# Kernel tuning notes

Measured on AMD Instinct MI355X. Metric: run time of the kernel, lower is better.

## Reference

```python
import jax, jax.numpy as jnp
import numpy as np

N_NODES = 100000
N_HYPEREDGES = 20000
NNZ = 600000
D = 128


def setup_inputs() -> dict:
    key = jax.random.key(0)
    k = jax.random.split(key, 6)
    s = 1.0 / np.sqrt(D)
    x = jax.random.normal(k[0], (N_NODES, D), jnp.float32)
    node_idx = jax.random.randint(k[1], (NNZ,), 0, N_NODES, dtype=jnp.int64 if jax.config.jax_enable_x64 else jnp.int32)
    edge_idx = jax.random.randint(k[2], (NNZ,), 0, N_HYPEREDGES, dtype=jnp.int64 if jax.config.jax_enable_x64 else jnp.int32)
    conv_W = jax.random.uniform(k[3], (D, D), jnp.float32, -s, s)
    conv_b = jnp.zeros((D,), jnp.float32)
    res_W = jax.random.uniform(k[4], (D, D), jnp.float32, -s, s)
    res_b = jax.random.uniform(k[5], (D,), jnp.float32, -s, s)
    return {"x": x, "node_idx": node_idx, "edge_idx": edge_idx,
            "conv_W": conv_W, "conv_b": conv_b, "res_W": res_W, "res_b": res_b}


def hypergraph_conv(x, node_idx, edge_idx, W, b):
    # PyG HypergraphConv (no attention, unit hyperedge weights):
    #   out = D^{-1} H B^{-1} H^T (x W) + b
    y = x @ W                                                      # [N, D]
    ones = jnp.ones(node_idx.shape, dtype=y.dtype)
    deg_n = jax.ops.segment_sum(ones, node_idx, num_segments=N_NODES)        # node degree
    deg_e = jax.ops.segment_sum(ones, edge_idx, num_segments=N_HYPEREDGES)   # hyperedge size
    inv_n = jnp.where(deg_n > 0, 1.0 / deg_n, 0.0)
    inv_e = jnp.where(deg_e > 0, 1.0 / deg_e, 0.0)
    # node -> hyperedge aggregation, normalized by B^{-1}
    e_feat = jax.ops.segment_sum(y[node_idx], edge_idx, num_segments=N_HYPEREDGES)
    e_feat = e_feat * inv_e[:, None]                               # [E, D]
    # hyperedge -> node aggregation, normalized by D^{-1}
    out = jax.ops.segment_sum(e_feat[edge_idx], node_idx, num_segments=N_NODES)
    out = out * inv_n[:, None]                                     # [N, D]
    return out + b


def reference(x, node_idx, edge_idx, conv_W, conv_b, res_W, res_b):
    h = hypergraph_conv(x, node_idx, edge_idx, conv_W, conv_b)     # layer_num = 1
    return (x @ res_W + res_b) + h                                 # residual Linear + conv out
```

## Files before the change

kernel.cpp:

```cpp
#include <hip/hip_runtime.h>

#define N_NODES 100000
#define N_EDGES 20000
#define NNZ_C   600000
#define D 128

typedef short bf16x8 __attribute__((ext_vector_type(8)));
typedef float f32x4  __attribute__((ext_vector_type(4)));

__device__ __forceinline__ unsigned short f2bf(float f) {
    unsigned int u = __float_as_uint(f);
    u = (u + 0x7fffu + ((u >> 16) & 1u)) >> 16;
    return (unsigned short)u;
}
__device__ __forceinline__ float bf2f(unsigned short h) {
    return __uint_as_float((unsigned int)h << 16);
}
__device__ __forceinline__ unsigned int pk_trunc(float lo, float hi) {
    return __builtin_amdgcn_perm(__float_as_uint(hi), __float_as_uint(lo),
                                 0x07060302);
}

#define CH 4096
#define NCHUNK 147
#define CONVB 256
#define EBW 32
#define NBE 625
#define ECAP 1280
#define NBW 128
#define NBN 782
#define NCAP 1024
#define PADI 32
#define GCUR_INTS ((NBE + NBN) * PADI)

#define GT 64
#define XPAD 136
#define NTILES ((N_NODES + GT - 1) / GT)

__global__ __launch_bounds__(512) void fused_bin_conv(
    const float* __restrict__ x,
    const int* __restrict__ nidx, const int* __restrict__ eidx,
    unsigned short* __restrict__ xb,
    int* __restrict__ bucket_e, int* __restrict__ bucket_n,
    int* __restrict__ gcur_e, int* __restrict__ gcur_n) {
    __shared__ int srt[CH];
    __shared__ int cnt[NBN], lbase[NBN], gbase[NBN], cur[NBN];
    const int bid = blockIdx.x;
    const int tid = threadIdx.x;

    if (bid >= NCHUNK) {
        const int total8 = N_NODES * D / 8;
        for (int g = (bid - NCHUNK) * 512 + tid; g < total8;
             g += CONVB * 512) {
            const float4 a = *(const float4*)(x + (size_t)g * 8);
            const float4 c = *(const float4*)(x + (size_t)g * 8 + 4);
            uint4 v;
            v.x = pk_trunc(a.x, a.y);
            v.y = pk_trunc(a.z, a.w);
            v.z = pk_trunc(c.x, c.y);
            v.w = pk_trunc(c.z, c.w);
            *(uint4*)(xb + (size_t)g * 8) = v;
        }
        return;
    }

    const int j0 = bid * CH;
    const int jn = (j0 + CH < NNZ_C) ? CH : NNZ_C - j0;
#pragma unroll
    for (int s = 0; s < 2; ++s) {
        const int nb = s ? NBN : NBE;
        int* gc = s ? gcur_n : gcur_e;
        int* dst = s ? bucket_n : bucket_e;
        const int cap = s ? NCAP : ECAP;
        for (int i = tid; i < nb; i += 512) cnt[i] = 0;
        __syncthreads();
        for (int i = tid; i < jn; i += 512) {
            const int id = s ? nidx[j0 + i] : eidx[j0 + i];
            atomicAdd(&cnt[s ? (id >> 7) : (id >> 5)], 1);
        }
        __syncthreads();
        if (tid < 64) {
            int loc[13];
            int ssum = 0;
            const int k0 = tid * 13;
#pragma unroll
            for (int k = 0; k < 13; ++k) {
                const int idx = k0 + k;
                loc[k] = ssum;
                if (idx < nb) ssum += cnt[idx];
            }
            int v = ssum;
#pragma unroll
            for (int off = 1; off < 64; off <<= 1) {
                const int t = __shfl_up(v, off);
                if (tid >= off) v += t;
            }
            const int base = v - ssum;
#pragma unroll
            for (int k = 0; k < 13; ++k) {
                const int idx = k0 + k;
                if (idx < nb) {
                    lbase[idx] = base + loc[k];
                    cur[idx] = base + loc[k];
                }
            }
        }
        __syncthreads();
        for (int i = tid; i < nb; i += 512)
            gbase[i] = cnt[i] ? atomicAdd(&gc[i * PADI], cnt[i]) : 0;
        __syncthreads();
        for (int i = tid; i < jn; i += 512) {
            const int e = eidx[j0 + i], n = nidx[j0 + i];
            const int b = s ? (n >> 7) : (e >> 5);
            const unsigned pk = s ? (unsigned)(((n & 127) << 15) | e)
                                  : (unsigned)(((e & 31) << 17) | n);
            const int pos = atomicAdd(&cur[b], 1);
            srt[pos] = (int)(pk | ((unsigned)b << 22));
        }
        __syncthreads();
        for (int i = tid; i < jn; i += 512) {
            const unsigned v = (unsigned)srt[i];
            const int b = v >> 22;
            const int o2 = gbase[b] + (i - lbase[b]);
            if (o2 < cap) dst[b * cap + o2] = (int)(v & 0x3FFFFFu);
        }
        __syncthreads();
    }
}

__global__ __launch_bounds__(512) void edge_mean(
    const int* __restrict__ bucket_e, const int* __restrict__ gcur_e,
    const unsigned short* __restrict__ xb, unsigned short* __restrict__ sb) {
    __shared__ int raw[ECAP];
    __shared__ int srt[ECAP];
    __shared__ int cnt[EBW + 1];
    __shared__ int cur[EBW];
    const int tid = threadIdx.x;
    const int b = blockIdx.x;
    int W = gcur_e[b * PADI];
    if (W > ECAP) W = ECAP;
    if (tid <= EBW) cnt[tid] = 0;
    __syncthreads();
    const int* src = bucket_e + b * ECAP;
    for (int i = tid; i < W; i += 512) {
        const int p = src[i];
        raw[i] = p;
        atomicAdd(&cnt[p >> 17], 1);
    }
    __syncthreads();
    if (tid < EBW) {
        const int c = cnt[tid];
        int v = c;
#pragma unroll
        for (int off = 1; off < EBW; off <<= 1) {
            const int t = __shfl_up(v, off);
            if (tid >= off) v += t;
        }
        cnt[tid] = v - c;
        cur[tid] = v - c;
        if (tid == EBW - 1) cnt[EBW] = v;
    }
    __syncthreads();
    for (int i = tid; i < W; i += 512) {
        const int p = raw[i];
        const int pos = atomicAdd(&cur[p >> 17], 1);
        srt[pos] = p & 0x1FFFF;
    }
    __syncthreads();

    const int g = tid >> 4;
    const int l = tid & 15;
    const int beg = cnt[g], end = cnt[g + 1];
    float acc[8] = {};
    int j = beg;
    for (; j + 8 <= end; j += 8) {
        bf16x8 p[8];
#pragma unroll
        for (int q = 0; q < 8; ++q)
            p[q] = *(const bf16x8*)(xb + (size_t)srt[j + q] * D + l * 8);
#pragma unroll
        for (int i = 0; i < 8; ++i) {
            float t0 = bf2f((unsigned short)p[0][i]) + bf2f((unsigned short)p[1][i]);
            float t1 = bf2f((unsigned short)p[2][i]) + bf2f((unsigned short)p[3][i]);
            float t2 = bf2f((unsigned short)p[4][i]) + bf2f((unsigned short)p[5][i]);
            float t3 = bf2f((unsigned short)p[6][i]) + bf2f((unsigned short)p[7][i]);
            acc[i] += (t0 + t1) + (t2 + t3);
        }
    }
    for (; j + 4 <= end; j += 4) {
        const int n0 = srt[j], n1 = srt[j + 1];
        const int n2 = srt[j + 2], n3 = srt[j + 3];
        const bf16x8 p0 = *(const bf16x8*)(xb + (size_t)n0 * D + l * 8);
        const bf16x8 p1 = *(const bf16x8*)(xb + (size_t)n1 * D + l * 8);
        const bf16x8 p2 = *(const bf16x8*)(xb + (size_t)n2 * D + l * 8);
        const bf16x8 p3 = *(const bf16x8*)(xb + (size_t)n3 * D + l * 8);
#pragma unroll
        for (int i = 0; i < 8; ++i)
            acc[i] += (bf2f((unsigned short)p0[i]) + bf2f((unsigned short)p1[i]))
                    + (bf2f((unsigned short)p2[i]) + bf2f((unsigned short)p3[i]));
    }
    for (; j < end; ++j) {
        const bf16x8 p = *(const bf16x8*)(xb + (size_t)srt[j] * D + l * 8);
#pragma unroll
        for (int i = 0; i < 8; ++i) acc[i] += bf2f((unsigned short)p[i]);
    }
    const int deg = end - beg;
    const float inv = deg ? 1.f / (float)deg : 0.f;
    bf16x8 o;
#pragma unroll
    for (int i = 0; i < 8; ++i) o[i] = (short)f2bf(acc[i] * inv);
    *(bf16x8*)(sb + (size_t)(b * EBW + g) * D + l * 8) = o;
}

__global__ __launch_bounds__(512, 4) void node_gemm(
    const int* __restrict__ bucket_n, const int* __restrict__ gcur_n,
    const unsigned short* __restrict__ sb, const unsigned short* __restrict__ xb,
    const float* __restrict__ cW, const float* __restrict__ rW,
    const float* __restrict__ cbias, const float* __restrict__ rbias,
    float* __restrict__ out) {
    __shared__ int raw[NCAP];
    __shared__ int srt[NCAP];
    __shared__ int cnt[NBW + 1];
    __shared__ int cur[NBW];
    __shared__ unsigned short zs[NBW * XPAD];
    __shared__ unsigned short xs[GT * XPAD];
    const int tid = threadIdx.x;
    const int b = blockIdx.x;

    int W = gcur_n[b * PADI];
    if (W > NCAP) W = NCAP;
    if (tid <= NBW) cnt[tid] = 0;
    __syncthreads();
    const int* src = bucket_n + b * NCAP;
    for (int i = tid; i < W; i += 512) {
        const int p = src[i];
        raw[i] = p;
        atomicAdd(&cnt[p >> 15], 1);
    }
    __syncthreads();
    if (tid < 64) {
        const int a0 = cnt[tid * 2], a1 = cnt[tid * 2 + 1];
        const int ssum = a0 + a1;
        int v = ssum;
#pragma unroll
        for (int off = 1; off < 64; off <<= 1) {
            const int t = __shfl_up(v, off);
            if (tid >= off) v += t;
        }
        const int base = v - ssum;
        cnt[tid * 2] = base;          cur[tid * 2] = base;
        cnt[tid * 2 + 1] = base + a0; cur[tid * 2 + 1] = base + a0;
        if (tid == 63) cnt[NBW] = v;
    }
    __syncthreads();
    for (int i = tid; i < W; i += 512) {
        const int p = raw[i];
        const int pos = atomicAdd(&cur[p >> 15], 1);
        srt[pos] = p & 0x7FFF;
    }
    __syncthreads();

    {
        const int g = tid >> 4;
        const int l = tid & 15;
#pragma unroll
        for (int u = 0; u < 4; ++u) {
            const int nl = g * 4 + u;
            const int beg = cnt[nl], end = cnt[nl + 1];
            float acc[8] = {};
            int j = beg;
            for (; j + 4 <= end; j += 4) {
                const int e0 = srt[j], e1 = srt[j + 1];
                const int e2 = srt[j + 2], e3 = srt[j + 3];
                const bf16x8 p0 = *(const bf16x8*)(sb + (size_t)e0 * D + l * 8);
                const bf16x8 p1 = *(const bf16x8*)(sb + (size_t)e1 * D + l * 8);
                const bf16x8 p2 = *(const bf16x8*)(sb + (size_t)e2 * D + l * 8);
                const bf16x8 p3 = *(const bf16x8*)(sb + (size_t)e3 * D + l * 8);
#pragma unroll
                for (int i = 0; i < 8; ++i)
                    acc[i] += (bf2f((unsigned short)p0[i]) + bf2f((unsigned short)p1[i]))
                            + (bf2f((unsigned short)p2[i]) + bf2f((unsigned short)p3[i]));
            }
            for (; j < end; ++j) {
                const bf16x8 p = *(const bf16x8*)(sb + (size_t)srt[j] * D + l * 8);
#pragma unroll
                for (int i = 0; i < 8; ++i) acc[i] += bf2f((unsigned short)p[i]);
            }
            const int deg = end - beg;
            const float inv = deg ? 1.f / (float)deg : 0.f;
            bf16x8 o;
#pragma unroll
            for (int i = 0; i < 8; ++i) o[i] = (short)f2bf(acc[i] * inv);
            *(bf16x8*)(zs + nl * XPAD + l * 8) = o;
        }
    }

    const int w    = tid >> 6;
    const int lane = tid & 63;
    const int quad = lane >> 4;
    const int l16  = lane & 15;
    const int f0   = w * 16;
    const int f    = f0 + l16;
    bf16x8 Ac[4], Ar[4];
#pragma unroll
    for (int kc = 0; kc < 4; ++kc)
#pragma unroll
        for (int u = 0; u < 8; ++u) {
            const int k = kc * 32 + quad * 8 + u;
            Ac[kc][u] = (short)f2bf(cW[(size_t)k * D + f]);
            Ar[kc][u] = (short)f2bf(rW[(size_t)k * D + f]);
        }
    const float4 cb4 = *(const float4*)(cbias + f0 + quad * 4);
    const float4 rb4 = *(const float4*)(rbias + f0 + quad * 4);
    const float4 bias = {cb4.x + rb4.x, cb4.y + rb4.y,
                         cb4.z + rb4.z, cb4.w + rb4.w};

    const int r0 = tid >> 3;
    const int qp = tid & 7;

#pragma unroll
    for (int h = 0; h < 2; ++h) {
        __syncthreads();
        {
            int n = b * NBW + h * GT + r0;
            if (n >= N_NODES) n = N_NODES - 1;
            const uint4* sx = (const uint4*)(xb + (size_t)n * D + qp * 16);
            uint4* dx = (uint4*)(xs + r0 * XPAD + qp * 16);
            dx[0] = sx[0]; dx[1] = sx[1];
        }
        __syncthreads();
        f32x4 acc[4] = {};
#pragma unroll
        for (int g = 0; g < 4; ++g)
#pragma unroll
            for (int kc = 0; kc < 4; ++kc) {
                const int ko = kc * 32 + quad * 8;
                const bf16x8 Bz = *(const bf16x8*)(zs + (h * GT + g * 16 + l16) * XPAD + ko);
                const bf16x8 Bx = *(const bf16x8*)(xs + (g * 16 + l16) * XPAD + ko);
                acc[g] = __builtin_amdgcn_mfma_f32_16x16x32_bf16(Ac[kc], Bz, acc[g], 0, 0, 0);
                acc[g] = __builtin_amdgcn_mfma_f32_16x16x32_bf16(Ar[kc], Bx, acc[g], 0, 0, 0);
            }
#pragma unroll
        for (int g = 0; g < 4; ++g) {
            const int n = b * NBW + h * GT + g * 16 + l16;
            if (n >= N_NODES) continue;
            float4 o;
            o.x = acc[g][0] + bias.x;
            o.y = acc[g][1] + bias.y;
            o.z = acc[g][2] + bias.z;
            o.w = acc[g][3] + bias.w;
            *(float4*)(out + (size_t)n * D + f0 + quad * 4) = o;
        }
    }
}

extern "C" void kernel_launch(void* const* d_in, const int* in_sizes, int n_in,
                              void* d_out, int out_size, void* d_ws,
                              size_t ws_size, hipStream_t stream) {
    const float* x  = (const float*)d_in[0];
    const int* nidx = (const int*)d_in[1];
    const int* eidx = (const int*)d_in[2];
    const float* cW = (const float*)d_in[3];
    const float* cb = (const float*)d_in[4];
    const float* rW = (const float*)d_in[5];
    const float* rb = (const float*)d_in[6];
    float* out = (float*)d_out;

    char* ws = (char*)d_ws;
    size_t off = 0;
    auto alloc = [&](size_t bytes) {
        size_t o = off;
        off += (bytes + 255) & ~(size_t)255;
        return o;
    };
    unsigned short* xb = (unsigned short*)(ws + alloc((size_t)N_NODES * D * 2));
    unsigned short* sb = (unsigned short*)(ws + alloc((size_t)N_EDGES * D * 2));
    int* bucket_e = (int*)(ws + alloc((size_t)NBE * ECAP * 4));
    int* bucket_n = (int*)(ws + alloc((size_t)NBN * NCAP * 4));
    int* gcur     = (int*)(ws + alloc((size_t)GCUR_INTS * 4));
    int* gcur_e = gcur;
    int* gcur_n = gcur + NBE * PADI;

    hipMemsetAsync(gcur, 0, (size_t)GCUR_INTS * 4, stream);

    fused_bin_conv<<<NCHUNK + CONVB, 512, 0, stream>>>(
        x, nidx, eidx, xb, bucket_e, bucket_n, gcur_e, gcur_n);

    edge_mean<<<NBE, 512, 0, stream>>>(bucket_e, gcur_e, xb, sb);
    node_gemm<<<NBN, 512, 0, stream>>>(bucket_n, gcur_n, sb, xb,
                                       cW, rW, cb, rb, out);
}
```

Baseline: 190.7 us.

## Halve bucket widths, pre-transpose bf16 weights, drop LDS raw staging

Bucket widths are halved: 16 hyperedges per edge bucket and 64 nodes per node bucket. This doubles the number of blocks in edge_mean and node_gemm, gives more parallelism and smaller LDS footprints, and lets node_gemm process a single 64-row tile. Extra blocks in the fused binning kernel convert and transpose both weight matrices to bf16 once, so each node_gemm block loads its MFMA A fragments with vector loads instead of 64 strided scalar fp32 loads. The raw LDS staging of bucket entries is removed, and bucket entries are re-read from global memory instead. The costs are a second global read of bucket data, more blocks re-loading weights, and tighter per-bucket capacities that risk truncation.

```diff
diff --git a/kernel.cpp b/kernel.cpp
--- a/kernel.cpp
+++ b/kernel.cpp
@@ -24,23 +24,27 @@
 #define CH 4096
 #define NCHUNK 147
 #define CONVB 256
-#define EBW 32
-#define NBE 625
-#define ECAP 1280
-#define NBW 128
-#define NBN 782
-#define NCAP 1024
+#define WBLK 8
+#define EBW 16
+#define NBE 1250
+#define ECAP 768
+#define NBW 64
+#define NBN 1563
+#define NCAP 640
 #define PADI 32
 #define GCUR_INTS ((NBE + NBN) * PADI)
+#define TAGSH 21
+#define PKMASK 0x1FFFFF
 
 #define GT 64
 #define XPAD 136
-#define NTILES ((N_NODES + GT - 1) / GT)
 
 __global__ __launch_bounds__(512) void fused_bin_conv(
     const float* __restrict__ x,
     const int* __restrict__ nidx, const int* __restrict__ eidx,
+    const float* __restrict__ cW, const float* __restrict__ rW,
     unsigned short* __restrict__ xb,
+    unsigned short* __restrict__ wtc, unsigned short* __restrict__ wtr,
     int* __restrict__ bucket_e, int* __restrict__ bucket_n,
     int* __restrict__ gcur_e, int* __restrict__ gcur_n) {
     __shared__ int srt[CH];
@@ -48,6 +52,18 @@
     const int bid = blockIdx.x;
     const int tid = threadIdx.x;
 
+    if (bid >= NCHUNK + CONVB) {
+        const int t0 = (bid - NCHUNK - CONVB) * 4096;
+        for (int i = tid; i < 4096; i += 512) {
+            const int t = t0 + i;
+            const int m = t >> 14, idx = t & 16383;
+            const int f = idx & 127, k = idx >> 7;
+            const float* src = m ? rW : cW;
+            unsigned short* dst = m ? wtr : wtc;
+            dst[f * D + k] = f2bf(src[k * D + f]);
+        }
+        return;
+    }
     if (bid >= NCHUNK) {
         const int total8 = N_NODES * D / 8;
         for (int g = (bid - NCHUNK) * 512 + tid; g < total8;
@@ -76,15 +92,15 @@
         __syncthreads();
         for (int i = tid; i < jn; i += 512) {
             const int id = s ? nidx[j0 + i] : eidx[j0 + i];
-            atomicAdd(&cnt[s ? (id >> 7) : (id >> 5)], 1);
+            atomicAdd(&cnt[s ? (id >> 6) : (id >> 4)], 1);
         }
         __syncthreads();
         if (tid < 64) {
-            int loc[13];
+            int loc[25];
             int ssum = 0;
-            const int k0 = tid * 13;
-#pragma unroll
-            for (int k = 0; k < 13; ++k) {
+            const int k0 = tid * 25;
+#pragma unroll
+            for (int k = 0; k < 25; ++k) {
                 const int idx = k0 + k;
                 loc[k] = ssum;
                 if (idx < nb) ssum += cnt[idx];
@@ -97,7 +113,7 @@
             }
             const int base = v - ssum;
 #pragma unroll
-            for (int k = 0; k < 13; ++k) {
+            for (int k = 0; k < 25; ++k) {
                 const int idx = k0 + k;
                 if (idx < nb) {
                     lbase[idx] = base + loc[k];
@@ -111,27 +127,26 @@
         __syncthreads();
         for (int i = tid; i < jn; i += 512) {
             const int e = eidx[j0 + i], n = nidx[j0 + i];
-            const int b = s ? (n >> 7) : (e >> 5);
-            const unsigned pk = s ? (unsigned)(((n & 127) << 15) | e)
-                                  : (unsigned)(((e & 31) << 17) | n);
+            const int b = s ? (n >> 6) : (e >> 4);
+            const unsigned pk = s ? (unsigned)(((n & 63) << 15) | e)
+                                  : (unsigned)(((e & 15) << 17) | n);
             const int pos = atomicAdd(&cur[b], 1);
-            srt[pos] = (int)(pk | ((unsigned)b << 22));
+            srt[pos] = (int)(pk | ((unsigned)b << TAGSH));
         }
         __syncthreads();
         for (int i = tid; i < jn; i += 512) {
             const unsigned v = (unsigned)srt[i];
-            const int b = v >> 22;
+            const int b = (int)(v >> TAGSH);
             const int o2 = gbase[b] + (i - lbase[b]);
-            if (o2 < cap) dst[b * cap + o2] = (int)(v & 0x3FFFFFu);
-        }
-        __syncthreads();
-    }
-}
-
-__global__ __launch_bounds__(512) void edge_mean(
+            if (o2 < cap) dst[b * cap + o2] = (int)(v & PKMASK);
+        }
+        __syncthreads();
+    }
+}
+
+__global__ __launch_bounds__(256) void edge_mean(
     const int* __restrict__ bucket_e, const int* __restrict__ gcur_e,
     const unsigned short* __restrict__ xb, unsigned short* __restrict__ sb) {
-    __shared__ int raw[ECAP];
     __shared__ int srt[ECAP];
     __shared__ int cnt[EBW + 1];
     __shared__ int cur[EBW];
@@ -142,11 +157,8 @@
     if (tid <= EBW) cnt[tid] = 0;
     __syncthreads();
     const int* src = bucket_e + b * ECAP;
-    for (int i = tid; i < W; i += 512) {
-        const int p = src[i];
-        raw[i] = p;
-        atomicAdd(&cnt[p >> 17], 1);
-    }
+    for (int i = tid; i < W; i += 256)
+        atomicAdd(&cnt[src[i] >> 17], 1);
     __syncthreads();
     if (tid < EBW) {
         const int c = cnt[tid];
@@ -161,8 +173,8 @@
         if (tid == EBW - 1) cnt[EBW] = v;
     }
     __syncthreads();
-    for (int i = tid; i < W; i += 512) {
-        const int p = raw[i];
+    for (int i = tid; i < W; i += 256) {
+        const int p = src[i];
         const int pos = atomicAdd(&cur[p >> 17], 1);
         srt[pos] = p & 0x1FFFF;
     }
@@ -215,10 +227,9 @@
 __global__ __launch_bounds__(512, 4) void node_gemm(
     const int* __restrict__ bucket_n, const int* __restrict__ gcur_n,
     const unsigned short* __restrict__ sb, const unsigned short* __restrict__ xb,
-    const float* __restrict__ cW, const float* __restrict__ rW,
+    const unsigned short* __restrict__ wtc, const unsigned short* __restrict__ wtr,
     const float* __restrict__ cbias, const float* __restrict__ rbias,
     float* __restrict__ out) {
-    __shared__ int raw[NCAP];
     __shared__ int srt[NCAP];
     __shared__ int cnt[NBW + 1];
     __shared__ int cur[NBW];
@@ -232,29 +243,24 @@
     if (tid <= NBW) cnt[tid] = 0;
     __syncthreads();
     const int* src = bucket_n + b * NCAP;
-    for (int i = tid; i < W; i += 512) {
-        const int p = src[i];
-        raw[i] = p;
-        atomicAdd(&cnt[p >> 15], 1);
-    }
+    for (int i = tid; i < W; i += 512)
+        atomicAdd(&cnt[src[i] >> 15], 1);
     __syncthreads();
     if (tid < 64) {
-        const int a0 = cnt[tid * 2], a1 = cnt[tid * 2 + 1];
-        const int ssum = a0 + a1;
-        int v = ssum;
+        const int c = cnt[tid];
+        int v = c;
 #pragma unroll
         for (int off = 1; off < 64; off <<= 1) {
             const int t = __shfl_up(v, off);
             if (tid >= off) v += t;
         }
-        const int base = v - ssum;
-        cnt[tid * 2] = base;          cur[tid * 2] = base;
-        cnt[tid * 2 + 1] = base + a0; cur[tid * 2 + 1] = base + a0;
+        cnt[tid] = v - c;
+        cur[tid] = v - c;
         if (tid == 63) cnt[NBW] = v;
     }
     __syncthreads();
     for (int i = tid; i < W; i += 512) {
-        const int p = raw[i];
+        const int p = src[i];
         const int pos = atomicAdd(&cur[p >> 15], 1);
         srt[pos] = p & 0x7FFF;
     }
@@ -264,8 +270,8 @@
         const int g = tid >> 4;
         const int l = tid & 15;
 #pragma unroll
-        for (int u = 0; u < 4; ++u) {
-            const int nl = g * 4 + u;
+        for (int u = 0; u < 2; ++u) {
+            const int nl = g * 2 + u;
             const int beg = cnt[nl], end = cnt[nl + 1];
             float acc[8] = {};
             int j = beg;
@@ -303,54 +309,46 @@
     const int f    = f0 + l16;
     bf16x8 Ac[4], Ar[4];
 #pragma unroll
-    for (int kc = 0; kc < 4; ++kc)
-#pragma unroll
-        for (int u = 0; u < 8; ++u) {
-            const int k = kc * 32 + quad * 8 + u;
-            Ac[kc][u] = (short)f2bf(cW[(size_t)k * D + f]);
-            Ar[kc][u] = (short)f2bf(rW[(size_t)k * D + f]);
-        }
+    for (int kc = 0; kc < 4; ++kc) {
+        Ac[kc] = *(const bf16x8*)(wtc + (size_t)f * D + kc * 32 + quad * 8);
+        Ar[kc] = *(const bf16x8*)(wtr + (size_t)f * D + kc * 32 + quad * 8);
+    }
     const float4 cb4 = *(const float4*)(cbias + f0 + quad * 4);
     const float4 rb4 = *(const float4*)(rbias + f0 + quad * 4);
     const float4 bias = {cb4.x + rb4.x, cb4.y + rb4.y,
                          cb4.z + rb4.z, cb4.w + rb4.w};
 
-    const int r0 = tid >> 3;
-    const int qp = tid & 7;
-
-#pragma unroll
-    for (int h = 0; h < 2; ++h) {
-        __syncthreads();
-        {
-            int n = b * NBW + h * GT + r0;
-            if (n >= N_NODES) n = N_NODES - 1;
-            const uint4* sx = (const uint4*)(xb + (size_t)n * D + qp * 16);
-            uint4* dx = (uint4*)(xs + r0 * XPAD + qp * 16);
-            dx[0] = sx[0]; dx[1] = sx[1];
-        }
-        __syncthreads();
-        f32x4 acc[4] = {};
-#pragma unroll
-        for (int g = 0; g < 4; ++g)
-#pragma unroll
-            for (int kc = 0; kc < 4; ++kc) {
-                const int ko = kc * 32 + quad * 8;
-                const bf16x8 Bz = *(const bf16x8*)(zs + (h * GT + g * 16 + l16) * XPAD + ko);
-                const bf16x8 Bx = *(const bf16x8*)(xs + (g * 16 + l16) * XPAD + ko);
-                acc[g] = __builtin_amdgcn_mfma_f32_16x16x32_bf16(Ac[kc], Bz, acc[g], 0, 0, 0);
-                acc[g] = __builtin_amdgcn_mfma_f32_16x16x32_bf16(Ar[kc], Bx, acc[g], 0, 0, 0);
-            }
-#pragma unroll
-        for (int g = 0; g < 4; ++g) {
-            const int n = b * NBW + h * GT + g * 16 + l16;
-            if (n >= N_NODES) continue;
-            float4 o;
-            o.x = acc[g][0] + bias.x;
-            o.y = acc[g][1] + bias.y;
-            o.z = acc[g][2] + bias.z;
-            o.w = acc[g][3] + bias.w;
-            *(float4*)(out + (size_t)n * D + f0 + quad * 4) = o;
-        }
+    {
+        const int r0 = tid >> 3;
+        const int qp = tid & 7;
+        int n = b * NBW + r0;
+        if (n >= N_NODES) n = N_NODES - 1;
+        const uint4* sx = (const uint4*)(xb + (size_t)n * D + qp * 16);
+        uint4* dx = (uint4*)(xs + r0 * XPAD + qp * 16);
+        dx[0] = sx[0]; dx[1] = sx[1];
+    }
+    __syncthreads();
+    f32x4 acc[4] = {};
+#pragma unroll
+    for (int g = 0; g < 4; ++g)
+#pragma unroll
+        for (int kc = 0; kc < 4; ++kc) {
+            const int ro = (g * 16 + l16) * XPAD + kc * 32 + quad * 8;
+            const bf16x8 Bz = *(const bf16x8*)(zs + ro);
+            const bf16x8 Bx = *(const bf16x8*)(xs + ro);
+            acc[g] = __builtin_amdgcn_mfma_f32_16x16x32_bf16(Ac[kc], Bz, acc[g], 0, 0, 0);
+            acc[g] = __builtin_amdgcn_mfma_f32_16x16x32_bf16(Ar[kc], Bx, acc[g], 0, 0, 0);
+        }
+#pragma unroll
+    for (int g = 0; g < 4; ++g) {
+        const int n = b * NBW + g * 16 + l16;
+        if (n >= N_NODES) continue;
+        float4 o;
+        o.x = acc[g][0] + bias.x;
+        o.y = acc[g][1] + bias.y;
+        o.z = acc[g][2] + bias.z;
+        o.w = acc[g][3] + bias.w;
+        *(float4*)(out + (size_t)n * D + f0 + quad * 4) = o;
     }
 }
 
@@ -373,8 +371,10 @@
         off += (bytes + 255) & ~(size_t)255;
         return o;
     };
-    unsigned short* xb = (unsigned short*)(ws + alloc((size_t)N_NODES * D * 2));
-    unsigned short* sb = (unsigned short*)(ws + alloc((size_t)N_EDGES * D * 2));
+    unsigned short* xb  = (unsigned short*)(ws + alloc((size_t)N_NODES * D * 2));
+    unsigned short* sb  = (unsigned short*)(ws + alloc((size_t)N_EDGES * D * 2));
+    unsigned short* wtc = (unsigned short*)(ws + alloc((size_t)D * D * 2));
+    unsigned short* wtr = (unsigned short*)(ws + alloc((size_t)D * D * 2));
     int* bucket_e = (int*)(ws + alloc((size_t)NBE * ECAP * 4));
     int* bucket_n = (int*)(ws + alloc((size_t)NBN * NCAP * 4));
     int* gcur     = (int*)(ws + alloc((size_t)GCUR_INTS * 4));
@@ -383,10 +383,11 @@
 
     hipMemsetAsync(gcur, 0, (size_t)GCUR_INTS * 4, stream);
 
-    fused_bin_conv<<<NCHUNK + CONVB, 512, 0, stream>>>(
-        x, nidx, eidx, xb, bucket_e, bucket_n, gcur_e, gcur_n);
-
-    edge_mean<<<NBE, 512, 0, stream>>>(bucket_e, gcur_e, xb, sb);
+    fused_bin_conv<<<NCHUNK + CONVB + WBLK, 512, 0, stream>>>(
+        x, nidx, eidx, cW, rW, xb, wtc, wtr,
+        bucket_e, bucket_n, gcur_e, gcur_n);
+
+    edge_mean<<<NBE, 256, 0, stream>>>(bucket_e, gcur_e, xb, sb);
     node_gemm<<<NBN, 512, 0, stream>>>(bucket_n, gcur_n, sb, xb,
-                                       cW, rW, cb, rb, out);
-}
+                                       wtc, wtr, cb, rb, out);
+}
```

Result: no change. 192.5 us (+1.0%).
